# Kernel optimization log

Measured on AMD Instinct MI355X. Metric: run time of the kernel, lower is better.

## Reference

```python
import jax, jax.numpy as jnp
import numpy as np

HEADS, DK, DV, STRIDE = 8, 32, 32, 2
EPS = 1e-5

def dwconv(x, w, b, stride):
    # depthwise 3x3, padding 1; w: [C,1,3,3]
    y = jax.lax.conv_general_dilated(
        x, w, (stride, stride), ((1, 1), (1, 1)),
        dimension_numbers=("NCHW", "OIHW", "NCHW"),
        feature_group_count=x.shape[1])
    return y + b[None, :, None, None]

def setup_inputs() -> dict:
    key = jax.random.key(0)
    ks = jax.random.split(key, 16)
    B_, C, H, W = 8, 256, 56, 56
    hd = HEADS * DK
    s = lambda k, shp: (jax.random.normal(k, shp, jnp.float32) * 0.02)
    return {
        "x": jax.random.normal(ks[0], (B_, C, H, W), jnp.float32),
        "Wk_dw": s(ks[1], (C, 1, 3, 3)), "bk_dw": jnp.zeros((C,), jnp.float32),
        "Wv_dw": s(ks[2], (C, 1, 3, 3)), "bv_dw": jnp.zeros((C,), jnp.float32),
        "Wq": s(ks[3], (hd, C)), "bq": jnp.zeros((hd,), jnp.float32),
        "Wk": s(ks[4], (hd, C)), "bk": jnp.zeros((hd,), jnp.float32),
        "Wv": s(ks[5], (HEADS * DV, C)), "bv": jnp.zeros((HEADS * DV,), jnp.float32),
        "Wo": s(ks[6], (C, HEADS * DV)), "bo": jnp.zeros((C,), jnp.float32),
        "Bbias": s(ks[7], (1, HEADS, H * W, (H // STRIDE) * (W // STRIDE))),
    }

def reference(x, Wk_dw, bk_dw, Wv_dw, bv_dw, Wq, bq, Wk, bk, Wv, bv, Wo, bo, Bbias):
    b, c, h, w = x.shape
    xr = x.reshape(b, c, h * w).transpose(0, 2, 1)  # [b, hw, c]
    # F.layer_norm with normalized_shape=(b, hw, c): single mean/var over ALL elements
    mu = jnp.mean(xr)
    var = jnp.mean((xr - mu) ** 2)
    xn = (xr - mu) * jax.lax.rsqrt(var + EPS)
    q = (xn @ Wq.T + bq).reshape(b, h * w, HEADS, DK).transpose(0, 2, 1, 3)  # [b,H,hw,dk]
    ki = dwconv(x, Wk_dw, bk_dw, STRIDE)
    kh, kw = ki.shape[2], ki.shape[3]
    kf = ki.reshape(b, c, kh * kw).transpose(0, 2, 1)
    k = (kf @ Wk.T + bk).reshape(b, kh * kw, HEADS, DK).transpose(0, 2, 1, 3)
    vi = dwconv(x, Wv_dw, bv_dw, STRIDE)
    vf = vi.reshape(b, c, kh * kw).transpose(0, 2, 1)
    v = (vf @ Wv.T + bv).reshape(b, kh * kw, HEADS, DV).transpose(0, 2, 1, 3)
    attn = jnp.einsum("bhid,bhjd->bhij", q, k) * (DK ** -0.5) + Bbias
    attn = jax.nn.softmax(attn, axis=-1)
    res = jnp.einsum("bhij,bhjd->bhid", attn, v).transpose(0, 2, 1, 3)
    res = res.reshape(b, h * w, HEADS * DV)
    out = (res @ Wo.T + bo).reshape(b, c, h, w)  # faithful to original .view (no transpose)
    return out + x
```

## Files before the change

kernel.cpp:

```cpp
#include <hip/hip_runtime.h>

typedef unsigned short u16;
typedef unsigned int   u32;
typedef __attribute__((ext_vector_type(8))) short short8;
typedef __attribute__((ext_vector_type(4))) float f32x4;
typedef __attribute__((ext_vector_type(4))) unsigned short us4;

#define MFMA16(a, b, c) __builtin_amdgcn_mfma_f32_16x16x32_bf16((a), (b), (c), 0, 0, 0)

static constexpr int B_ = 8;
static constexpr int HW = 3136;
static constexpr int KW = 784;
static constexpr int NELEM = B_ * 256 * HW;
static constexpr int NBB = 8 * HW * KW;

static constexpr size_t OFF_CNT = 4096;
static constexpr size_t OFF_W   = 8192;
static constexpr int AOFF_WQ = 0, AOFF_WK = 65536, AOFF_WV = 131072, AOFF_WO = 196608;
static constexpr int AOFF_WKDW = 262144, AOFF_WVDW = 264448;
static constexpr int AOFF_BKDW = 266752, AOFF_BVDW = 267008, AOFF_BQ = 267264;
static constexpr int AOFF_BK = 267520, AOFF_BV = 267776, AOFF_BO = 268032;
static constexpr size_t OFF_XT  = 557056;
static constexpr size_t SZ_XT   = (size_t)B_ * HW * 256 * 2;
static constexpr size_t SZ_KJ   = (size_t)B_ * KW * 256 * 2;
static constexpr size_t OFF_KIT = OFF_XT + SZ_XT;
static constexpr size_t OFF_VIT = OFF_KIT + SZ_KJ;
static constexpr size_t OFF_KI  = OFF_VIT + SZ_KJ;
static constexpr size_t OFF_VI  = OFF_KI + SZ_KJ;
static constexpr size_t OFF_Q   = OFF_VI + SZ_KJ;
static constexpr size_t OFF_O   = OFF_XT;
static constexpr size_t OFF_BB  = OFF_Q + SZ_XT;
static constexpr size_t SZ_BB   = (size_t)NBB * 2;

__device__ __forceinline__ float bf2f(u16 u) { return __uint_as_float(((u32)u) << 16); }
__device__ __forceinline__ u16 f2bf(float f) {
  u32 u = __float_as_uint(f);
  u32 r = u + 0x7FFFu + ((u >> 16) & 1u);
  return (u16)(r >> 16);
}
__device__ __forceinline__ u32 cvtpk(float lo, float hi) {
  u32 r;
  asm("v_cvt_pk_bf16_f32 %0, %1, %2" : "=v"(r) : "v"(lo), "v"(hi));
  return r;
}

__global__ __launch_bounds__(256) void detect_k(const u32* __restrict__ x, int* __restrict__ cnt) {
  int c = 0;
  for (int i = threadIdx.x; i < 4096; i += 256) {
    float v = __uint_as_float(x[i] << 16);
    if (fabsf(v) > 1e4f) c++;
  }
#pragma unroll
  for (int off = 32; off > 0; off >>= 1) c += __shfl_down(c, off);
  if ((threadIdx.x & 63) == 0) atomicAdd(cnt, c);
}

struct CvtArgs { const void* src[12]; int dstoff[12]; int n[12]; };
__global__ __launch_bounds__(256) void cvtw_k(CvtArgs a, u16* __restrict__ arena,
                                              const int* __restrict__ cnt) {
  int t = blockIdx.y;
  int n = a.n[t];
  u16* d = arena + a.dstoff[t];
  int f32m = (*cnt >= 64);
  if (f32m) {
    const float* s = (const float*)a.src[t];
    for (int i = blockIdx.x * 256 + threadIdx.x; i < n; i += gridDim.x * 256) d[i] = f2bf(s[i]);
  } else {
    const u16* s = (const u16*)a.src[t];
    for (int i = blockIdx.x * 256 + threadIdx.x; i < n; i += gridDim.x * 256) d[i] = s[i];
  }
}

__global__ __launch_bounds__(256) void cvtb_k(const void* __restrict__ src, u16* __restrict__ dst,
                                              const int* __restrict__ cnt) {
  int f32m = (*cnt >= 64);
  const int n4 = NBB / 4;
  if (f32m) {
    const float4* s = (const float4*)src;
    us4* d = (us4*)dst;
    for (int i = blockIdx.x * 256 + threadIdx.x; i < n4; i += gridDim.x * 256) {
      float4 v = s[i];
      us4 o = {f2bf(v.x), f2bf(v.y), f2bf(v.z), f2bf(v.w)};
      d[i] = o;
    }
  } else {
    const uint2* s = (const uint2*)src;
    uint2* d = (uint2*)dst;
    for (int i = blockIdx.x * 256 + threadIdx.x; i < n4; i += gridDim.x * 256) d[i] = s[i];
  }
}

__global__ __launch_bounds__(256) void reduce_k(const void* __restrict__ x, double* __restrict__ acc,
                                                const int* __restrict__ cnt) {
  int f32m = (*cnt >= 64);
  float s = 0.f, ss = 0.f;
  if (f32m) {
    const float4* xv = (const float4*)x;
    const int n4 = NELEM / 4;
    for (int i = blockIdx.x * 256 + threadIdx.x; i < n4; i += gridDim.x * 256) {
      float4 u = xv[i];
      s += u.x + u.y + u.z + u.w;
      ss += u.x * u.x + u.y * u.y + u.z * u.z + u.w * u.w;
    }
  } else {
    const uint4* xv = (const uint4*)x;
    const int n8 = NELEM / 8;
    for (int i = blockIdx.x * 256 + threadIdx.x; i < n8; i += gridDim.x * 256) {
      uint4 u = xv[i];
      u32 w[4] = {u.x, u.y, u.z, u.w};
#pragma unroll
      for (int q = 0; q < 4; q++) {
        float f0 = __uint_as_float(w[q] << 16);
        float f1 = __uint_as_float(w[q] & 0xFFFF0000u);
        s += f0 + f1;
        ss += f0 * f0 + f1 * f1;
      }
    }
  }
#pragma unroll
  for (int off = 32; off > 0; off >>= 1) {
    s += __shfl_down(s, off);
    ss += __shfl_down(ss, off);
  }
  __shared__ float as_[4], ass_[4];
  int wv = threadIdx.x >> 6;
  if ((threadIdx.x & 63) == 0) { as_[wv] = s; ass_[wv] = ss; }
  __syncthreads();
  if (threadIdx.x == 0) {
    atomicAdd(acc + 0, (double)(as_[0] + as_[1] + as_[2] + as_[3]));
    atomicAdd(acc + 1, (double)(ass_[0] + ass_[1] + ass_[2] + ass_[3]));
  }
}

__global__ __launch_bounds__(256) void prep_k(const u16* __restrict__ wq, const u16* __restrict__ bq,
                                              float* __restrict__ wsf) {
  const double* acc = (const double*)wsf;
  __shared__ float sh[2];
  if (threadIdx.x == 0) {
    double N = (double)NELEM;
    double mu = acc[0] / N;
    double var = acc[1] / N - mu * mu;
    float rstd = (float)(1.0 / sqrt(var + 1e-5));
    sh[0] = (float)mu; sh[1] = rstd;
    wsf[4] = (float)mu; wsf[5] = rstd;
    wsf[6] = rstd * 0.17677669529663687f;
  }
  __syncthreads();
  int o = threadIdx.x;
  float wsum = 0.f;
  for (int c = 0; c < 256; c++) wsum += bf2f(wq[o * 256 + c]);
  wsf[16 + o] = (bf2f(bq[o]) - sh[1] * sh[0] * wsum) * 0.17677669529663687f;
}

__global__ __launch_bounds__(256) void transpose_x_k(const void* __restrict__ src, u16* __restrict__ dst,
                                                     const int* __restrict__ cnt) {
  int f32m = (*cnt >= 64);
  __shared__ u16 t[32][33];
  int b = blockIdx.z;
  int r0 = blockIdx.y * 32, c0 = blockIdx.x * 32;
  int tid = threadIdx.x, col = tid & 31;
  size_t base = (size_t)b * 256 * HW;
  if (f32m) {
    const float* s = (const float*)src + base;
#pragma unroll
    for (int i = 0; i < 4; i++) {
      int row = (tid >> 5) + i * 8;
      t[row][col] = f2bf(s[(size_t)(r0 + row) * HW + c0 + col]);
    }
  } else {
    const u16* s = (const u16*)src + base;
#pragma unroll
    for (int i = 0; i < 4; i++) {
      int row = (tid >> 5) + i * 8;
      t[row][col] = s[(size_t)(r0 + row) * HW + c0 + col];
    }
  }
  __syncthreads();
  u16* d = dst + base;
#pragma unroll
  for (int i = 0; i < 4; i++) {
    int row = (tid >> 5) + i * 8;
    d[(size_t)(c0 + row) * 256 + r0 + col] = t[col][row];
  }
}

__global__ __launch_bounds__(256) void transpose_k(const u16* __restrict__ src, u16* __restrict__ dst,
                                                   int R, int Cc) {
  __shared__ u16 t[32][33];
  int b = blockIdx.z;
  int r0 = blockIdx.y * 32, c0 = blockIdx.x * 32;
  const u16* s = src + (size_t)b * R * Cc;
  u16* d = dst + (size_t)b * R * Cc;
  int tid = threadIdx.x, col = tid & 31;
#pragma unroll
  for (int i = 0; i < 4; i++) {
    int row = (tid >> 5) + i * 8;
    if (r0 + row < R && c0 + col < Cc) t[row][col] = s[(size_t)(r0 + row) * Cc + c0 + col];
  }
  __syncthreads();
#pragma unroll
  for (int i = 0; i < 4; i++) {
    int row = (tid >> 5) + i * 8;
    if (c0 + row < Cc && r0 + col < R) d[(size_t)(c0 + row) * R + r0 + col] = t[col][row];
  }
}

__global__ __launch_bounds__(256) void dwconv_k(const void* __restrict__ x,
                                                const u16* __restrict__ arena,
                                                u16* __restrict__ ki, u16* __restrict__ vi,
                                                const int* __restrict__ cnt) {
  int f32m = (*cnt >= 64);
  int b = blockIdx.x >> 8;
  int c = blockIdx.x & 255;
  float wkf[9], wvf[9];
#pragma unroll
  for (int t = 0; t < 9; t++) {
    wkf[t] = bf2f(arena[AOFF_WKDW + c * 9 + t]);
    wvf[t] = bf2f(arena[AOFF_WVDW + c * 9 + t]);
  }
  float kb = bf2f(arena[AOFF_BKDW + c]), vb = bf2f(arena[AOFF_BVDW + c]);
  size_t xbase = (size_t)(b * 256 + c) * HW;
  auto body = [&](auto LDX) {
    for (int j = threadIdx.x; j < KW; j += 256) {
      int oi = j / 28, oj = j % 28;
      float ka = kb, va = vb;
#pragma unroll
      for (int di = 0; di < 3; di++) {
        int ii = 2 * oi - 1 + di;
        if ((unsigned)ii >= 56u) continue;
#pragma unroll
        for (int dj = 0; dj < 3; dj++) {
          int ij = 2 * oj - 1 + dj;
          if ((unsigned)ij >= 56u) continue;
          float xv = LDX(ii * 56 + ij);
          ka += xv * wkf[di * 3 + dj];
          va += xv * wvf[di * 3 + dj];
        }
      }
      ki[(size_t)(b * 256 + c) * KW + j] = f2bf(ka);
      vi[(size_t)(b * 256 + c) * KW + j] = f2bf(va);
    }
  };
  if (f32m) {
    const float* xp = (const float*)x + xbase;
    body([&](int i) { return xp[i]; });
  } else {
    const u16* xp = (const u16*)x + xbase;
    body([&](int i) { return bf2f(xp[i]); });
  }
}

__global__ __launch_bounds__(256) void proj_q_k(const u16* __restrict__ xt, const u16* __restrict__ Wq,
                                                const float* __restrict__ wsf, u16* __restrict__ q) {
  int lane = threadIdx.x & 63, wave = threadIdx.x >> 6;
  int l15 = lane & 15, quad = lane >> 4;
  int b = blockIdx.x / 49, pb = blockIdx.x % 49;
  int p0 = pb * 64 + wave * 16;
  const u16* arow = xt + ((size_t)(b * HW) + p0 + l15) * 256 + quad * 8;
  short8 af[8];
#pragma unroll
  for (int ks = 0; ks < 8; ks++) af[ks] = *(const short8*)(arow + ks * 32);
  float alpha = wsf[6];
  const float* beta = wsf + 16;
  for (int ot = 0; ot < 16; ot++) {
    const u16* brow = Wq + (size_t)(ot * 16 + l15) * 256 + quad * 8;
    f32x4 acc = {0.f, 0.f, 0.f, 0.f};
#pragma unroll
    for (int ks = 0; ks < 8; ks++) acc = MFMA16(af[ks], *(const short8*)(brow + ks * 32), acc);
    int o = ot * 16 + l15;
    float bet = beta[o];
    size_t base = ((size_t)(b * HW) + p0 + quad * 4) * 256 + o;
#pragma unroll
    for (int r = 0; r < 4; r++) q[base + (size_t)r * 256] = f2bf(alpha * acc[r] + bet);
  }
}

__global__ __launch_bounds__(256) void proj_k_k(const u16* __restrict__ kit, const u16* __restrict__ Wk,
                                                const u16* __restrict__ bk, u16* __restrict__ kout) {
  int lane = threadIdx.x & 63, wave = threadIdx.x >> 6;
  int l15 = lane & 15, quad = lane >> 4;
  int b = blockIdx.x / 13, jb = blockIdx.x % 13;
  int p0 = jb * 64 + wave * 16;
  if (p0 >= KW) return;
  const u16* arow = kit + ((size_t)(b * KW) + p0 + l15) * 256 + quad * 8;
  short8 af[8];
#pragma unroll
  for (int ks = 0; ks < 8; ks++) af[ks] = *(const short8*)(arow + ks * 32);
  for (int ot = 0; ot < 16; ot++) {
    const u16* brow = Wk + (size_t)(ot * 16 + l15) * 256 + quad * 8;
    f32x4 acc = {0.f, 0.f, 0.f, 0.f};
#pragma unroll
    for (int ks = 0; ks < 8; ks++) acc = MFMA16(af[ks], *(const short8*)(brow + ks * 32), acc);
    int o = ot * 16 + l15;
    float bias = bf2f(bk[o]);
    size_t base = ((size_t)(b * KW) + p0 + quad * 4) * 256 + o;
#pragma unroll
    for (int r = 0; r < 4; r++) kout[base + (size_t)r * 256] = f2bf(acc[r] + bias);
  }
}

__global__ __launch_bounds__(256) void proj_v_k(const u16* __restrict__ Wv, const u16* __restrict__ vit,
                                                const u16* __restrict__ bv, u16* __restrict__ vT) {
  int lane = threadIdx.x & 63, wave = threadIdx.x >> 6;
  int l15 = lane & 15, quad = lane >> 4;
  int b = blockIdx.x >> 4;
  int ob = (blockIdx.x >> 2) & 3;
  int js = blockIdx.x & 3;
  int o0 = ob * 64 + wave * 16;
  const u16* arow = Wv + (size_t)(o0 + l15) * 256 + quad * 8;
  short8 af[8];
#pragma unroll
  for (int ks = 0; ks < 8; ks++) af[ks] = *(const short8*)(arow + ks * 32);
  int jt0 = js * 13;
  int jt1 = (jt0 + 13 < 49) ? jt0 + 13 : 49;
  for (int jt = jt0; jt < jt1; jt++) {
    const u16* brow = vit + ((size_t)(b * KW) + jt * 16 + l15) * 256 + quad * 8;
    f32x4 acc = {0.f, 0.f, 0.f, 0.f};
#pragma unroll
    for (int ks = 0; ks < 8; ks++) acc = MFMA16(af[ks], *(const short8*)(brow + ks * 32), acc);
#pragma unroll
    for (int r = 0; r < 4; r++) {
      int o = o0 + quad * 4 + r;
      vT[((size_t)(b * 256) + o) * KW + jt * 16 + l15] = f2bf(acc[r] + bf2f(bv[o]));
    }
  }
}

template <typename LD>
__device__ __forceinline__ void attn_body(const u16* __restrict__ qptr, const u16* __restrict__ kptr,
                                          const u16* __restrict__ vptr, u16* __restrict__ Ob,
                                          int b, int h, int p0, LD ldb) {
  int lane = threadIdx.x & 63;
  int l15 = lane & 15, quad = lane >> 4;
  const u16* qp = qptr + ((size_t)(b * HW) + p0 + l15) * 256 + h * 32 + quad * 8;
  short8 qf0 = *(const short8*)qp;
  short8 qf1 = *(const short8*)(qp + 16 * 256);
  const u16* kb = kptr + (size_t)b * KW * 256 + h * 32 + quad * 8;
  const u16* vb = vptr + ((size_t)(b * 256) + h * 32) * KW;
  const f32x4 zz = {0.f, 0.f, 0.f, 0.f};
  f32x4 o00 = zz, o01 = zz, o10 = zz, o11 = zz;
  float ls0 = 0.f, ls1 = 0.f;

  for (int jt = 0; jt < 49; jt++) {
    short8 kf = *(const short8*)(kb + (size_t)(jt * 16 + l15) * 256);
    f32x4 s0 = MFMA16(kf, qf0, zz);
    f32x4 s1 = MFMA16(kf, qf1, zz);
    f32x4 b0 = ldb(0, jt), b1 = ldb(1, jt);
    float e00 = __expf(fminf(s0[0] + b0[0], 30.f));
    float e01 = __expf(fminf(s0[1] + b0[1], 30.f));
    float e02 = __expf(fminf(s0[2] + b0[2], 30.f));
    float e03 = __expf(fminf(s0[3] + b0[3], 30.f));
    float e10 = __expf(fminf(s1[0] + b1[0], 30.f));
    float e11 = __expf(fminf(s1[1] + b1[1], 30.f));
    float e12 = __expf(fminf(s1[2] + b1[2], 30.f));
    float e13 = __expf(fminf(s1[3] + b1[3], 30.f));
    ls0 += (e00 + e01) + (e02 + e03);
    ls1 += (e10 + e11) + (e12 + e13);
    union { u32 u[4]; short8 s; } pa, pb;
    pa.u[0] = cvtpk(e00, e01); pa.u[1] = cvtpk(e02, e03); pa.u[2] = 0; pa.u[3] = 0;
    pb.u[0] = cvtpk(e10, e11); pb.u[1] = cvtpk(e12, e13); pb.u[2] = 0; pb.u[3] = 0;
    int jo = jt * 16 + quad * 4;
    uint2 va2 = *(const uint2*)(vb + (size_t)l15 * KW + jo);
    uint2 vb2 = *(const uint2*)(vb + (size_t)(16 + l15) * KW + jo);
    union { u32 u[4]; short8 s; } va, vbf;
    va.u[0] = va2.x;  va.u[1] = va2.y;  va.u[2] = 0; va.u[3] = 0;
    vbf.u[0] = vb2.x; vbf.u[1] = vb2.y; vbf.u[2] = 0; vbf.u[3] = 0;
    o00 = MFMA16(va.s, pa.s, o00);
    o01 = MFMA16(vbf.s, pa.s, o01);
    o10 = MFMA16(va.s, pb.s, o10);
    o11 = MFMA16(vbf.s, pb.s, o11);
  }
  ls0 += __shfl_xor(ls0, 16); ls0 += __shfl_xor(ls0, 32);
  ls1 += __shfl_xor(ls1, 16); ls1 += __shfl_xor(ls1, 32);
  float inv0 = 1.f / ls0, inv1 = 1.f / ls1;
  size_t ob0 = ((size_t)(b * HW) + p0 + l15) * 256 + h * 32 + quad * 4;
  us4 w0, w1, w2, w3;
#pragma unroll
  for (int r = 0; r < 4; r++) {
    w0[r] = f2bf(o00[r] * inv0);
    w1[r] = f2bf(o01[r] * inv0);
    w2[r] = f2bf(o10[r] * inv1);
    w3[r] = f2bf(o11[r] * inv1);
  }
  *(us4*)(Ob + ob0) = w0;
  *(us4*)(Ob + ob0 + 16) = w1;
  *(us4*)(Ob + ob0 + (size_t)16 * 256) = w2;
  *(us4*)(Ob + ob0 + (size_t)16 * 256 + 16) = w3;
}

template <int BMODE>
__global__ __launch_bounds__(256) void attn_k(const u16* __restrict__ q, const u16* __restrict__ k,
                                              const u16* __restrict__ vT, const void* __restrict__ Bb,
                                              u16* __restrict__ Ob, const int* __restrict__ cnt) {
  int lane = threadIdx.x & 63;
  int l15 = lane & 15, quad = lane >> 4;
  int task = blockIdx.x * 4 + (threadIdx.x >> 6);
  int pt = task % 98;
  int t = task / 98;
  int h = t & 7, b = t >> 3;
  int p0 = pt * 32;
  size_t bbase = ((size_t)(h * HW) + p0 + l15) * KW + quad * 4;
  if constexpr (BMODE == 0) {
    const u16* bb = (const u16*)Bb;
    attn_body(q, k, vT, Ob, b, h, p0, [&](int sub, int jt) -> f32x4 {
      us4 v = *(const us4*)(bb + bbase + (size_t)(sub * 16) * KW + jt * 16);
      f32x4 r = {bf2f(v[0]), bf2f(v[1]), bf2f(v[2]), bf2f(v[3])};
      return r;
    });
  } else {
    if (*cnt >= 64) {
      const float* bf = (const float*)Bb;
      attn_body(q, k, vT, Ob, b, h, p0, [&](int sub, int jt) -> f32x4 {
        float4 v = *(const float4*)(bf + bbase + (size_t)(sub * 16) * KW + jt * 16);
        f32x4 r = {v.x, v.y, v.z, v.w};
        return r;
      });
    } else {
      const u16* bb = (const u16*)Bb;
      attn_body(q, k, vT, Ob, b, h, p0, [&](int sub, int jt) -> f32x4 {
        us4 v = *(const us4*)(bb + bbase + (size_t)(sub * 16) * KW + jt * 16);
        f32x4 r = {bf2f(v[0]), bf2f(v[1]), bf2f(v[2]), bf2f(v[3])};
        return r;
      });
    }
  }
}

__global__ __launch_bounds__(256) void proj_o_k(const u16* __restrict__ Ob, const u16* __restrict__ Wo,
                                                const u16* __restrict__ bo, const void* __restrict__ x,
                                                void* __restrict__ out, const int* __restrict__ cnt) {
  int f32m = (*cnt >= 64);
  int lane = threadIdx.x & 63, wave = threadIdx.x >> 6;
  int l15 = lane & 15, quad = lane >> 4;
  int b = blockIdx.x / 49, pb = blockIdx.x % 49;
  int p0 = pb * 64 + wave * 16;
  const u16* arow = Ob + ((size_t)(b * HW) + p0 + l15) * 256 + quad * 8;
  short8 af[8];
#pragma unroll
  for (int ks = 0; ks < 8; ks++) af[ks] = *(const short8*)(arow + ks * 32);
  for (int ot = 0; ot < 16; ot++) {
    const u16* brow = Wo + (size_t)(ot * 16 + l15) * 256 + quad * 8;
    f32x4 acc = {0.f, 0.f, 0.f, 0.f};
#pragma unroll
    for (int ks = 0; ks < 8; ks++) acc = MFMA16(af[ks], *(const short8*)(brow + ks * 32), acc);
    int o = ot * 16 + l15;
    float bias = bf2f(bo[o]);
    if (f32m) {
      const float* xf = (const float*)x;
      float* of = (float*)out;
#pragma unroll
      for (int r = 0; r < 4; r++) {
        size_t idx = ((size_t)(b * HW) + p0 + quad * 4 + r) * 256 + o;
        of[idx] = acc[r] + bias + xf[idx];
      }
    } else {
      const u16* xb = (const u16*)x;
      u16* ob_ = (u16*)out;
#pragma unroll
      for (int r = 0; r < 4; r++) {
        size_t idx = ((size_t)(b * HW) + p0 + quad * 4 + r) * 256 + o;
        ob_[idx] = f2bf(acc[r] + bias + bf2f(xb[idx]));
      }
    }
  }
}

extern "C" void kernel_launch(void* const* d_in, const int* in_sizes, int n_in,
                              void* d_out, int out_size, void* d_ws, size_t ws_size,
                              hipStream_t stream) {
  (void)in_sizes; (void)n_in; (void)out_size;
  const void* x = d_in[0];
  char* ws = (char*)d_ws;
  int* cnt = (int*)(ws + OFF_CNT);
  u16* arena = (u16*)(ws + OFF_W);
  u16* xt  = (u16*)(ws + OFF_XT);
  u16* kit = (u16*)(ws + OFF_KIT);
  u16* vit = (u16*)(ws + OFF_VIT);
  u16* ki  = (u16*)(ws + OFF_KI);
  u16* vi  = (u16*)(ws + OFF_VI);
  u16* qb  = (u16*)(ws + OFF_Q);
  u16* Obuf = (u16*)(ws + OFF_O);
  u16* bbA = (u16*)(ws + OFF_BB);
  bool big_ws = ws_size >= (OFF_BB + SZ_BB);

  CvtArgs a;
  const int srcidx[12] = {5, 7, 9, 11, 1, 3, 2, 4, 6, 8, 10, 12};
  const int dofs[12] = {AOFF_WQ, AOFF_WK, AOFF_WV, AOFF_WO, AOFF_WKDW, AOFF_WVDW,
                        AOFF_BKDW, AOFF_BVDW, AOFF_BQ, AOFF_BK, AOFF_BV, AOFF_BO};
  const int ns[12] = {65536, 65536, 65536, 65536, 2304, 2304, 256, 256, 256, 256, 256, 256};
  for (int i = 0; i < 12; i++) { a.src[i] = d_in[srcidx[i]]; a.dstoff[i] = dofs[i]; a.n[i] = ns[i]; }

  hipMemsetAsync(d_ws, 0, 8192, stream);
  detect_k<<<1, 256, 0, stream>>>((const u32*)x, cnt);
  cvtw_k<<<dim3(32, 12), 256, 0, stream>>>(a, arena, cnt);
  if (big_ws) cvtb_k<<<2048, 256, 0, stream>>>(d_in[13], bbA, cnt);
  reduce_k<<<1024, 256, 0, stream>>>(x, (double*)d_ws, cnt);
  prep_k<<<1, 256, 0, stream>>>(arena + AOFF_WQ, arena + AOFF_BQ, (float*)d_ws);
  transpose_x_k<<<dim3(98, 8, 8), 256, 0, stream>>>(x, xt, cnt);
  dwconv_k<<<2048, 256, 0, stream>>>(x, arena, ki, vi, cnt);
  transpose_k<<<dim3(25, 8, 8), 256, 0, stream>>>(ki, kit, 256, KW);
  transpose_k<<<dim3(25, 8, 8), 256, 0, stream>>>(vi, vit, 256, KW);
  proj_k_k<<<104, 256, 0, stream>>>(kit, arena + AOFF_WK, arena + AOFF_BK, ki);
  proj_v_k<<<128, 256, 0, stream>>>(arena + AOFF_WV, vit, arena + AOFF_BV, vi);
  proj_q_k<<<392, 256, 0, stream>>>(xt, arena + AOFF_WQ, (const float*)d_ws, qb);
  if (big_ws) attn_k<0><<<1568, 256, 0, stream>>>(qb, ki, vi, bbA, Obuf, cnt);
  else        attn_k<1><<<1568, 256, 0, stream>>>(qb, ki, vi, d_in[13], Obuf, cnt);
  proj_o_k<<<392, 256, 0, stream>>>(Obuf, arena + AOFF_WO, arena + AOFF_BO, x, d_out, cnt);
}
```

Measured before the change: 479.5 us.

## Fuse dwconv with transpose, merge K/V projections and conversion launches

The depthwise conv now writes its outputs directly in channel-last layout (one thread per channel, one block per output row), which removes the two separate transpose kernels. The K and V projection kernels are merged into one launch dispatched by block index, and the weight and bias conversion kernels are combined into one launch. The goal is fewer launches and less intermediate traffic. The cost is that the new dwconv uses only 224 blocks, and each thread walks a strided column of x, so its loads across a wave are spread out by channel stride and coalesce poorly.

```diff
diff --git a/kernel.cpp b/kernel.cpp
--- a/kernel.cpp
+++ b/kernel.cpp
@@ -56,37 +56,39 @@
 }
 
 struct CvtArgs { const void* src[12]; int dstoff[12]; int n[12]; };
-__global__ __launch_bounds__(256) void cvtw_k(CvtArgs a, u16* __restrict__ arena,
-                                              const int* __restrict__ cnt) {
-  int t = blockIdx.y;
+__global__ __launch_bounds__(256) void cvt_all_k(CvtArgs a, u16* __restrict__ arena,
+                                                 const void* __restrict__ bsrc,
+                                                 u16* __restrict__ bdst, int bias_blocks,
+                                                 const int* __restrict__ cnt) {
+  int f32m = (*cnt >= 64);
+  int bid = blockIdx.x;
+  if (bid < bias_blocks) {
+    const int n4 = NBB / 4;
+    if (f32m) {
+      const float4* s = (const float4*)bsrc;
+      us4* d = (us4*)bdst;
+      for (int i = bid * 256 + threadIdx.x; i < n4; i += bias_blocks * 256) {
+        float4 v = s[i];
+        us4 o = {f2bf(v.x), f2bf(v.y), f2bf(v.z), f2bf(v.w)};
+        d[i] = o;
+      }
+    } else {
+      const uint2* s = (const uint2*)bsrc;
+      uint2* d = (uint2*)bdst;
+      for (int i = bid * 256 + threadIdx.x; i < n4; i += bias_blocks * 256) d[i] = s[i];
+    }
+    return;
+  }
+  int wb = bid - bias_blocks;
+  int t = wb >> 2, sub = wb & 3;
   int n = a.n[t];
   u16* d = arena + a.dstoff[t];
-  int f32m = (*cnt >= 64);
   if (f32m) {
     const float* s = (const float*)a.src[t];
-    for (int i = blockIdx.x * 256 + threadIdx.x; i < n; i += gridDim.x * 256) d[i] = f2bf(s[i]);
+    for (int i = sub * 256 + threadIdx.x; i < n; i += 1024) d[i] = f2bf(s[i]);
   } else {
     const u16* s = (const u16*)a.src[t];
-    for (int i = blockIdx.x * 256 + threadIdx.x; i < n; i += gridDim.x * 256) d[i] = s[i];
-  }
-}
-
-__global__ __launch_bounds__(256) void cvtb_k(const void* __restrict__ src, u16* __restrict__ dst,
-                                              const int* __restrict__ cnt) {
-  int f32m = (*cnt >= 64);
-  const int n4 = NBB / 4;
-  if (f32m) {
-    const float4* s = (const float4*)src;
-    us4* d = (us4*)dst;
-    for (int i = blockIdx.x * 256 + threadIdx.x; i < n4; i += gridDim.x * 256) {
-      float4 v = s[i];
-      us4 o = {f2bf(v.x), f2bf(v.y), f2bf(v.z), f2bf(v.w)};
-      d[i] = o;
-    }
-  } else {
-    const uint2* s = (const uint2*)src;
-    uint2* d = (uint2*)dst;
-    for (int i = blockIdx.x * 256 + threadIdx.x; i < n4; i += gridDim.x * 256) d[i] = s[i];
+    for (int i = sub * 256 + threadIdx.x; i < n; i += 1024) d[i] = s[i];
   }
 }
 
@@ -184,34 +186,14 @@
   }
 }
 
-__global__ __launch_bounds__(256) void transpose_k(const u16* __restrict__ src, u16* __restrict__ dst,
-                                                   int R, int Cc) {
-  __shared__ u16 t[32][33];
-  int b = blockIdx.z;
-  int r0 = blockIdx.y * 32, c0 = blockIdx.x * 32;
-  const u16* s = src + (size_t)b * R * Cc;
-  u16* d = dst + (size_t)b * R * Cc;
-  int tid = threadIdx.x, col = tid & 31;
-#pragma unroll
-  for (int i = 0; i < 4; i++) {
-    int row = (tid >> 5) + i * 8;
-    if (r0 + row < R && c0 + col < Cc) t[row][col] = s[(size_t)(r0 + row) * Cc + c0 + col];
-  }
-  __syncthreads();
-#pragma unroll
-  for (int i = 0; i < 4; i++) {
-    int row = (tid >> 5) + i * 8;
-    if (c0 + row < Cc && r0 + col < R) d[(size_t)(c0 + row) * R + r0 + col] = t[col][row];
-  }
-}
-
-__global__ __launch_bounds__(256) void dwconv_k(const void* __restrict__ x,
-                                                const u16* __restrict__ arena,
-                                                u16* __restrict__ ki, u16* __restrict__ vi,
-                                                const int* __restrict__ cnt) {
+__global__ __launch_bounds__(256) void dwconv_t_k(const void* __restrict__ x,
+                                                  const u16* __restrict__ arena,
+                                                  u16* __restrict__ kit, u16* __restrict__ vit,
+                                                  const int* __restrict__ cnt) {
   int f32m = (*cnt >= 64);
-  int b = blockIdx.x >> 8;
-  int c = blockIdx.x & 255;
+  int bid = blockIdx.x;
+  int b = bid / 28, oi = bid % 28;
+  int c = threadIdx.x;
   float wkf[9], wvf[9];
 #pragma unroll
   for (int t = 0; t < 9; t++) {
@@ -221,8 +203,7 @@
   float kb = bf2f(arena[AOFF_BKDW + c]), vb = bf2f(arena[AOFF_BVDW + c]);
   size_t xbase = (size_t)(b * 256 + c) * HW;
   auto body = [&](auto LDX) {
-    for (int j = threadIdx.x; j < KW; j += 256) {
-      int oi = j / 28, oj = j % 28;
+    for (int oj = 0; oj < 28; oj++) {
       float ka = kb, va = vb;
 #pragma unroll
       for (int di = 0; di < 3; di++) {
@@ -237,8 +218,9 @@
           va += xv * wvf[di * 3 + dj];
         }
       }
-      ki[(size_t)(b * 256 + c) * KW + j] = f2bf(ka);
-      vi[(size_t)(b * 256 + c) * KW + j] = f2bf(va);
+      size_t o = ((size_t)b * KW + oi * 28 + oj) * 256 + c;
+      kit[o] = f2bf(ka);
+      vit[o] = f2bf(va);
     }
   };
   if (f32m) {
@@ -275,11 +257,12 @@
   }
 }
 
-__global__ __launch_bounds__(256) void proj_k_k(const u16* __restrict__ kit, const u16* __restrict__ Wk,
-                                                const u16* __restrict__ bk, u16* __restrict__ kout) {
+__device__ __forceinline__ void proj_k_body(int bid, const u16* __restrict__ kit,
+                                            const u16* __restrict__ Wk, const u16* __restrict__ bk,
+                                            u16* __restrict__ kout) {
   int lane = threadIdx.x & 63, wave = threadIdx.x >> 6;
   int l15 = lane & 15, quad = lane >> 4;
-  int b = blockIdx.x / 13, jb = blockIdx.x % 13;
+  int b = bid / 13, jb = bid % 13;
   int p0 = jb * 64 + wave * 16;
   if (p0 >= KW) return;
   const u16* arow = kit + ((size_t)(b * KW) + p0 + l15) * 256 + quad * 8;
@@ -298,14 +281,14 @@
     for (int r = 0; r < 4; r++) kout[base + (size_t)r * 256] = f2bf(acc[r] + bias);
   }
 }
-
-__global__ __launch_bounds__(256) void proj_v_k(const u16* __restrict__ Wv, const u16* __restrict__ vit,
-                                                const u16* __restrict__ bv, u16* __restrict__ vT) {
+__device__ __forceinline__ void proj_v_body(int bid, const u16* __restrict__ Wv,
+                                            const u16* __restrict__ vit, const u16* __restrict__ bv,
+                                            u16* __restrict__ vT) {
   int lane = threadIdx.x & 63, wave = threadIdx.x >> 6;
   int l15 = lane & 15, quad = lane >> 4;
-  int b = blockIdx.x >> 4;
-  int ob = (blockIdx.x >> 2) & 3;
-  int js = blockIdx.x & 3;
+  int b = bid >> 4;
+  int ob = (bid >> 2) & 3;
+  int js = bid & 3;
   int o0 = ob * 64 + wave * 16;
   const u16* arow = Wv + (size_t)(o0 + l15) * 256 + quad * 8;
   short8 af[8];
@@ -324,6 +307,14 @@
       vT[((size_t)(b * 256) + o) * KW + jt * 16 + l15] = f2bf(acc[r] + bf2f(bv[o]));
     }
   }
+}
+__global__ __launch_bounds__(256) void projkv_k(const u16* __restrict__ kit, const u16* __restrict__ Wk,
+                                                const u16* __restrict__ bk, u16* __restrict__ kout,
+                                                const u16* __restrict__ vit, const u16* __restrict__ Wv,
+                                                const u16* __restrict__ bv, u16* __restrict__ vT) {
+  int bid = blockIdx.x;
+  if (bid < 104) proj_k_body(bid, kit, Wk, bk, kout);
+  else           proj_v_body(bid - 104, Wv, vit, bv, vT);
 }
 
 template <typename LD>
@@ -492,16 +483,14 @@
 
   hipMemsetAsync(d_ws, 0, 8192, stream);
   detect_k<<<1, 256, 0, stream>>>((const u32*)x, cnt);
-  cvtw_k<<<dim3(32, 12), 256, 0, stream>>>(a, arena, cnt);
-  if (big_ws) cvtb_k<<<2048, 256, 0, stream>>>(d_in[13], bbA, cnt);
+  int bias_blocks = big_ws ? 2048 : 0;
+  cvt_all_k<<<bias_blocks + 48, 256, 0, stream>>>(a, arena, d_in[13], bbA, bias_blocks, cnt);
   reduce_k<<<1024, 256, 0, stream>>>(x, (double*)d_ws, cnt);
   prep_k<<<1, 256, 0, stream>>>(arena + AOFF_WQ, arena + AOFF_BQ, (float*)d_ws);
   transpose_x_k<<<dim3(98, 8, 8), 256, 0, stream>>>(x, xt, cnt);
-  dwconv_k<<<2048, 256, 0, stream>>>(x, arena, ki, vi, cnt);
-  transpose_k<<<dim3(25, 8, 8), 256, 0, stream>>>(ki, kit, 256, KW);
-  transpose_k<<<dim3(25, 8, 8), 256, 0, stream>>>(vi, vit, 256, KW);
-  proj_k_k<<<104, 256, 0, stream>>>(kit, arena + AOFF_WK, arena + AOFF_BK, ki);
-  proj_v_k<<<128, 256, 0, stream>>>(arena + AOFF_WV, vit, arena + AOFF_BV, vi);
+  dwconv_t_k<<<224, 256, 0, stream>>>(x, arena, kit, vit, cnt);
+  projkv_k<<<232, 256, 0, stream>>>(kit, arena + AOFF_WK, arena + AOFF_BK, ki,
+                                    vit, arena + AOFF_WV, arena + AOFF_BV, vi);
   proj_q_k<<<392, 256, 0, stream>>>(xt, arena + AOFF_WQ, (const float*)d_ws, qb);
   if (big_ws) attn_k<0><<<1568, 256, 0, stream>>>(qb, ki, vi, bbA, Obuf, cnt);
   else        attn_k<1><<<1568, 256, 0, stream>>>(qb, ki, vi, d_in[13], Obuf, cnt);
```

Result: no change. 480.2 us (+0.1%).
